# Optimization experiments

Measured on AMD Instinct MI355X. Metric: run time of the kernel, lower is better.

Reference implementation:

```python
import jax, jax.numpy as jnp
import numpy as np

N = 50000
E = 400000
IN_C = 512
HID = 64
OUT_C = 40
H = 4
NEG_SLOPE = 0.2
EPS = 1e-16  # PyG softmax denominator epsilon


def glorot(key, shape, fan_in, fan_out):
    limit = float(np.sqrt(6.0 / (fan_in + fan_out)))
    return jax.random.uniform(key, shape, jnp.float32, -limit, limit)


def setup_inputs() -> dict:
    key = jax.random.key(0)
    ks = jax.random.split(key, 8)
    x = jax.random.normal(ks[0], (N, IN_C), jnp.float32)
    # random edges guaranteed to have src != dst (forward adds exactly one self-loop per node)
    src = jax.random.randint(ks[1], (E,), 0, N)
    off = jax.random.randint(ks[2], (E,), 1, N)
    dst = (src + off) % N
    edge_index = jnp.stack([src, dst], axis=0).astype(jnp.int64)
    W1 = glorot(ks[3], (IN_C, H * HID), IN_C, H * HID)
    b1 = jnp.zeros((H * HID,), jnp.float32)
    W2 = glorot(ks[4], (H * HID, H * OUT_C), H * HID, H * OUT_C)
    b2 = jnp.zeros((OUT_C,), jnp.float32)
    return {"x": x, "edge_index": edge_index, "W1": W1, "b1": b1, "W2": W2, "b2": b2}


def _supergat_layer(x, src, dst, W, b, heads, out_c, concat):
    n = x.shape[0]
    h = (x @ W).reshape(n, heads, out_c)            # [N,H,C]
    x_i = h[dst]                                    # [E',H,C] target
    x_j = h[src]                                    # [E',H,C] source
    # MX attention with return_logits=True inside message(): plain dot-product logits
    alpha = jnp.sum(x_i * x_j, axis=-1)             # [E',H]
    alpha = jax.nn.leaky_relu(alpha, NEG_SLOPE)
    # segment softmax over destination node
    amax = jax.ops.segment_max(alpha, dst, num_segments=n)
    alpha = jnp.exp(alpha - amax[dst])
    denom = jax.ops.segment_sum(alpha, dst, num_segments=n)
    alpha = alpha / (denom[dst] + EPS)
    out = jax.ops.segment_sum(x_j * alpha[:, :, None], dst, num_segments=n)  # [N,H,C]
    if concat:
        out = out.reshape(n, heads * out_c)
    else:
        out = out.mean(axis=1)
    return out + b


def reference(x, edge_index, W1, b1, W2, b2):
    # add_self_loops (input edges contain no self loops by construction)
    loop = jnp.arange(N, dtype=edge_index.dtype)
    src = jnp.concatenate([edge_index[0], loop])
    dst = jnp.concatenate([edge_index[1], loop])
    h = _supergat_layer(x, src, dst, W1, b1, H, HID, concat=True)
    h = jax.nn.elu(h)
    out = _supergat_layer(h, src, dst, W2, b2, H, OUT_C, concat=False)
    logp = jax.nn.log_softmax(out, axis=-1)
    att_loss = jnp.zeros((1,), jnp.float32)  # eval mode: get_attention_loss returns 0
    return logp, att_loss
```

## Files before the change

kernel.cpp:

```cpp
#include <hip/hip_runtime.h>
#include <cstddef>
#include <cstdint>

#define HEADS 4
#define OUTC  40
#define NEG   0.2f
#define EPSV  1e-16f

typedef __bf16 bf16x8 __attribute__((ext_vector_type(8)));
typedef float  floatx4 __attribute__((ext_vector_type(4)));

__device__ __forceinline__ void split_bf16(float a, unsigned& hi, unsigned& lo) {
  unsigned u = __float_as_uint(a);
  hi = u >> 16;
  float hf = __uint_as_float(u & 0xFFFF0000u);
  lo = __float_as_uint(a - hf) >> 16;
}

__device__ __forceinline__ void dma16(const void* g, void* l) {
  __builtin_amdgcn_global_load_lds(
      (const __attribute__((address_space(1))) unsigned int*)g,
      (__attribute__((address_space(3))) unsigned int*)l, 16, 0, 0);
}

__global__ void hist_k(const int* __restrict__ dst, int* __restrict__ cnt, int E) {
  int e = blockIdx.x * blockDim.x + threadIdx.x;
  if (e < E) atomicAdd(&cnt[dst[e]], 1);
}

__global__ __launch_bounds__(1024) void scanA_k(const int* __restrict__ cnt,
                                                int* __restrict__ rp,
                                                int* __restrict__ bsum, int n) {
  __shared__ int sh[1024];
  int i = blockIdx.x * 1024 + threadIdx.x;
  int v = (i < n) ? cnt[i] : 0;
  sh[threadIdx.x] = v;
  __syncthreads();
  for (int d = 1; d < 1024; d <<= 1) {
    int t = (threadIdx.x >= d) ? sh[threadIdx.x - d] : 0;
    __syncthreads();
    sh[threadIdx.x] += t;
    __syncthreads();
  }
  if (i < n) rp[i] = sh[threadIdx.x] - v;
  if (threadIdx.x == 1023) bsum[blockIdx.x] = sh[1023];
}

__global__ void scanC_k(int* __restrict__ rp, const int* __restrict__ bsum,
                        int n, int nb) {
  int i = blockIdx.x * blockDim.x + threadIdx.x;
  if (i < n) {
    int b = i >> 10;
    int off = 0;
    for (int j = 0; j < b; ++j) off += bsum[j];
    rp[i] += off;
  }
  if (i == 0) {
    int tot = 0;
    for (int j = 0; j < nb; ++j) tot += bsum[j];
    rp[n] = tot;
  }
}

__global__ void scatter_k(const int* __restrict__ src, const int* __restrict__ dst,
                          const int* __restrict__ rp, int* __restrict__ cur,
                          int* __restrict__ out, int E) {
  int e = blockIdx.x * blockDim.x + threadIdx.x;
  if (e < E) {
    int d = dst[e];
    int p = rp[d] + atomicAdd(&cur[d], 1);
    out[p] = src[e];
  }
}

__global__ void convW_k(const float* __restrict__ W1, unsigned short* __restrict__ Wh1,
                        unsigned short* __restrict__ Wl1,
                        const float* __restrict__ W2, unsigned short* __restrict__ Wh2,
                        unsigned short* __restrict__ Wl2) {
  int id = blockIdx.x * 256 + threadIdx.x;
  if (id < 256 * 512) {
    int n = id >> 9, k = id & 511;
    unsigned h, l;
    split_bf16(W1[k * 256 + n], h, l);
    Wh1[id] = (unsigned short)h;
    Wl1[id] = (unsigned short)l;
  } else {
    int id2 = id - 256 * 512;
    int n = id2 >> 8, k = id2 & 255;
    int hh = n >> 6, c = n & 63;
    float a = (c < OUTC) ? W2[k * 160 + hh * OUTC + c] : 0.f;
    unsigned h, l;
    split_bf16(a, h, l);
    Wh2[id2] = (unsigned short)h;
    Wl2[id2] = (unsigned short)l;
  }
}

template <bool A_FP32, bool COMPACT>
__global__ __launch_bounds__(256, 3) void gemm_dma(const void* Aptr_h, const void* Aptr_l,
                                                   const unsigned short* __restrict__ Bh,
                                                   const unsigned short* __restrict__ Bl,
                                                   float* __restrict__ C, int M, int K) {
  __shared__ __align__(16) unsigned char lds[49152];
  const int tid = threadIdx.x;
  const int lane = tid & 63;
  const int w = tid >> 6;
  const int wr = w >> 1, wc = w & 1;
  const int row0 = blockIdx.y * 128;
  const int col0 = blockIdx.x * 128;
  const int fr = lane & 15, fq = lane >> 4;
  const int swz8 = fr & 7;
  const int swz4 = (fr & 3) ^ ((fr >> 2) & 1);
  const int srcA8 = (lane & 7) ^ (lane >> 3);
  const int srcB4 = (lane & 3) ^ ((lane >> 2) & 3) ^ ((lane >> 4) & 1);

  floatx4 acc[4][4];
#pragma unroll
  for (int i = 0; i < 4; ++i)
#pragma unroll
    for (int j = 0; j < 4; ++j) acc[i][j] = (floatx4){0.f, 0.f, 0.f, 0.f};

  const float* Af32 = (const float*)Aptr_h;
  const unsigned short* Agh = (const unsigned short*)Aptr_h;
  const unsigned short* Agl = (const unsigned short*)Aptr_l;

#define DMA_A(K0)                                                                   \
  do {                                                                              \
    if (A_FP32) {                                                                   \
      _Pragma("unroll") for (int t = 0; t < 4; ++t) {                               \
        int arow = w * 32 + t * 8 + (lane >> 3);                                    \
        int gr = row0 + arow; gr = gr < M ? gr : M - 1;                             \
        dma16(&Af32[(size_t)gr * K + (K0) + srcA8 * 4],                             \
              lds + (size_t)(w * 32 + t * 8) * 128);                                \
      }                                                                             \
    } else {                                                                        \
      _Pragma("unroll") for (int t = 0; t < 2; ++t) {                               \
        int arow = w * 32 + t * 16 + (lane >> 2);                                   \
        int gr = row0 + arow; gr = gr < M ? gr : M - 1;                             \
        size_t go = (size_t)gr * K + (K0) + srcB4 * 8;                              \
        dma16(&Agh[go], lds + (size_t)(w * 32 + t * 16) * 64);                      \
        dma16(&Agl[go], lds + 8192 + (size_t)(w * 32 + t * 16) * 64);               \
      }                                                                             \
    }                                                                               \
  } while (0)

#define DMA_B(K0, BASE)                                                             \
  do {                                                                              \
    _Pragma("unroll") for (int t = 0; t < 2; ++t) {                                 \
      int nrow = w * 32 + t * 16 + (lane >> 2);                                     \
      size_t go = (size_t)(col0 + nrow) * K + (K0) + srcB4 * 8;                     \
      dma16(&Bh[go], lds + (BASE) + (size_t)(w * 32 + t * 16) * 64);                \
      dma16(&Bl[go], lds + (BASE) + 8192 + (size_t)(w * 32 + t * 16) * 64);         \
    }                                                                               \
  } while (0)

  const int nk = K >> 5;
  DMA_B(0, 16384);
  DMA_A(0);
  asm volatile("" ::: "memory");
  for (int k = 0; k < nk; ++k) {
    const int bbase = 16384 + ((k & 1) << 14);
    if (k + 1 < nk) {
      DMA_B((k + 1) << 5, 16384 + (((k + 1) & 1) << 14));
      asm volatile("s_waitcnt vmcnt(4)" ::: "memory");
    } else {
      asm volatile("s_waitcnt vmcnt(0)" ::: "memory");
    }
    asm volatile("s_barrier" ::: "memory");

    bf16x8 ah[4], al[4], bh[4], bl[4];
#pragma unroll
    for (int i = 0; i < 4; ++i) {
      int arow = wr * 64 + i * 16 + fr;
      if (A_FP32) {
        const unsigned char* pa = lds + (size_t)arow * 128;
        float4 v0 = *(const float4*)(pa + (((fq * 2) ^ swz8) * 16));
        float4 v1 = *(const float4*)(pa + (((fq * 2 + 1) ^ swz8) * 16));
        unsigned u0 = __float_as_uint(v0.x), u1 = __float_as_uint(v0.y);
        unsigned u2 = __float_as_uint(v0.z), u3 = __float_as_uint(v0.w);
        unsigned u4 = __float_as_uint(v1.x), u5 = __float_as_uint(v1.y);
        unsigned u6 = __float_as_uint(v1.z), u7 = __float_as_uint(v1.w);
        uint4 H;
        H.x = (u0 >> 16) | (u1 & 0xFFFF0000u);
        H.y = (u2 >> 16) | (u3 & 0xFFFF0000u);
        H.z = (u4 >> 16) | (u5 & 0xFFFF0000u);
        H.w = (u6 >> 16) | (u7 & 0xFFFF0000u);
        uint4 L;
        L.x = (__float_as_uint(v0.x - __uint_as_float(u0 & 0xFFFF0000u)) >> 16) |
              (__float_as_uint(v0.y - __uint_as_float(u1 & 0xFFFF0000u)) & 0xFFFF0000u);
        L.y = (__float_as_uint(v0.z - __uint_as_float(u2 & 0xFFFF0000u)) >> 16) |
              (__float_as_uint(v0.w - __uint_as_float(u3 & 0xFFFF0000u)) & 0xFFFF0000u);
        L.z = (__float_as_uint(v1.x - __uint_as_float(u4 & 0xFFFF0000u)) >> 16) |
              (__float_as_uint(v1.y - __uint_as_float(u5 & 0xFFFF0000u)) & 0xFFFF0000u);
        L.w = (__float_as_uint(v1.z - __uint_as_float(u6 & 0xFFFF0000u)) >> 16) |
              (__float_as_uint(v1.w - __uint_as_float(u7 & 0xFFFF0000u)) & 0xFFFF0000u);
        ah[i] = *(bf16x8*)&H;
        al[i] = *(bf16x8*)&L;
      } else {
        ah[i] = *(bf16x8*)(lds + (size_t)arow * 64 + ((fq ^ swz4) * 16));
        al[i] = *(bf16x8*)(lds + 8192 + (size_t)arow * 64 + ((fq ^ swz4) * 16));
      }
      int brow = wc * 64 + i * 16 + fr;
      bh[i] = *(bf16x8*)(lds + bbase + (size_t)brow * 64 + ((fq ^ swz4) * 16));
      bl[i] = *(bf16x8*)(lds + bbase + 8192 + (size_t)brow * 64 + ((fq ^ swz4) * 16));
    }
    asm volatile("s_waitcnt lgkmcnt(0)" ::: "memory");
    asm volatile("s_barrier" ::: "memory");
    if (k + 1 < nk) DMA_A((k + 1) << 5);

#pragma unroll
    for (int i = 0; i < 4; ++i)
#pragma unroll
      for (int j = 0; j < 4; ++j) {
        acc[i][j] = __builtin_amdgcn_mfma_f32_16x16x32_bf16(ah[i], bh[j], acc[i][j], 0, 0, 0);
        acc[i][j] = __builtin_amdgcn_mfma_f32_16x16x32_bf16(ah[i], bl[j], acc[i][j], 0, 0, 0);
        acc[i][j] = __builtin_amdgcn_mfma_f32_16x16x32_bf16(al[i], bh[j], acc[i][j], 0, 0, 0);
      }
  }
#undef DMA_A
#undef DMA_B

#pragma unroll
  for (int i = 0; i < 4; ++i) {
    int grow_base = row0 + wr * 64 + i * 16 + fq * 4;
#pragma unroll
    for (int r = 0; r < 4; ++r) {
      int grow = grow_base + r;
      if (grow < M) {
        if (COMPACT) {
          int head = blockIdx.x * 2 + wc;
#pragma unroll
          for (int j = 0; j < 4; ++j) {
            int cc = j * 16 + fr;
            if (cc < OUTC) C[(size_t)grow * 160 + head * OUTC + cc] = acc[i][j][r];
          }
        } else {
#pragma unroll
          for (int j = 0; j < 4; ++j)
            C[(size_t)grow * 256 + col0 + wc * 64 + j * 16 + fr] = acc[i][j][r];
        }
      }
    }
  }
}

__global__ __launch_bounds__(256) void agg1_k(const float* __restrict__ h,
                                              const int* __restrict__ rp,
                                              const int* __restrict__ srt,
                                              const float* __restrict__ b1,
                                              unsigned short* __restrict__ outh,
                                              unsigned short* __restrict__ outl, int Nn) {
  int wv = threadIdx.x >> 6, lane = threadIdx.x & 63;
  int node = blockIdx.x * 4 + wv;
  if (node >= Nn) node = Nn - 1;
  const float4 xi = *(const float4*)&h[(size_t)node * 256 + lane * 4];
  float p = xi.x * xi.x + xi.y * xi.y + xi.z * xi.z + xi.w * xi.w;
  p += __shfl_xor(p, 1); p += __shfl_xor(p, 2); p += __shfl_xor(p, 4); p += __shfl_xor(p, 8);
  float a = p > 0.f ? p : NEG * p;
  float m = a, l = 1.f;
  float4 acc = xi;
  const int e0 = rp[node], e1 = rp[node + 1];
  int e = e0;
  for (; e + 4 <= e1; e += 4) {
    int s0 = srt[e], s1 = srt[e + 1], s2 = srt[e + 2], s3 = srt[e + 3];
    const float4 xj0 = *(const float4*)&h[(size_t)s0 * 256 + lane * 4];
    const float4 xj1 = *(const float4*)&h[(size_t)s1 * 256 + lane * 4];
    const float4 xj2 = *(const float4*)&h[(size_t)s2 * 256 + lane * 4];
    const float4 xj3 = *(const float4*)&h[(size_t)s3 * 256 + lane * 4];
    float q0 = xi.x * xj0.x + xi.y * xj0.y + xi.z * xj0.z + xi.w * xj0.w;
    float q1 = xi.x * xj1.x + xi.y * xj1.y + xi.z * xj1.z + xi.w * xj1.w;
    float q2 = xi.x * xj2.x + xi.y * xj2.y + xi.z * xj2.z + xi.w * xj2.w;
    float q3 = xi.x * xj3.x + xi.y * xj3.y + xi.z * xj3.z + xi.w * xj3.w;
    q0 += __shfl_xor(q0, 1); q1 += __shfl_xor(q1, 1); q2 += __shfl_xor(q2, 1); q3 += __shfl_xor(q3, 1);
    q0 += __shfl_xor(q0, 2); q1 += __shfl_xor(q1, 2); q2 += __shfl_xor(q2, 2); q3 += __shfl_xor(q3, 2);
    q0 += __shfl_xor(q0, 4); q1 += __shfl_xor(q1, 4); q2 += __shfl_xor(q2, 4); q3 += __shfl_xor(q3, 4);
    q0 += __shfl_xor(q0, 8); q1 += __shfl_xor(q1, 8); q2 += __shfl_xor(q2, 8); q3 += __shfl_xor(q3, 8);
    float a0 = q0 > 0.f ? q0 : NEG * q0;
    float a1 = q1 > 0.f ? q1 : NEG * q1;
    float a2 = q2 > 0.f ? q2 : NEG * q2;
    float a3 = q3 > 0.f ? q3 : NEG * q3;
    float nm = fmaxf(fmaxf(m, fmaxf(a0, a1)), fmaxf(a2, a3));
    float sc = __expf(m - nm);
    float w0 = __expf(a0 - nm), w1 = __expf(a1 - nm);
    float w2 = __expf(a2 - nm), w3 = __expf(a3 - nm);
    l = l * sc + w0 + w1 + w2 + w3;
    acc.x = acc.x * sc + w0 * xj0.x + w1 * xj1.x + w2 * xj2.x + w3 * xj3.x;
    acc.y = acc.y * sc + w0 * xj0.y + w1 * xj1.y + w2 * xj2.y + w3 * xj3.y;
    acc.z = acc.z * sc + w0 * xj0.z + w1 * xj1.z + w2 * xj2.z + w3 * xj3.z;
    acc.w = acc.w * sc + w0 * xj0.w + w1 * xj1.w + w2 * xj2.w + w3 * xj3.w;
    m = nm;
  }
  for (; e < e1; ++e) {
    int s = srt[e];
    const float4 xj = *(const float4*)&h[(size_t)s * 256 + lane * 4];
    float q = xi.x * xj.x + xi.y * xj.y + xi.z * xj.z + xi.w * xj.w;
    q += __shfl_xor(q, 1); q += __shfl_xor(q, 2); q += __shfl_xor(q, 4); q += __shfl_xor(q, 8);
    float al = q > 0.f ? q : NEG * q;
    float nm = fmaxf(m, al);
    float sc = __expf(m - nm), wt = __expf(al - nm);
    l = l * sc + wt;
    acc.x = acc.x * sc + wt * xj.x;
    acc.y = acc.y * sc + wt * xj.y;
    acc.z = acc.z * sc + wt * xj.z;
    acc.w = acc.w * sc + wt * xj.w;
    m = nm;
  }
  float inv = 1.f / (l + EPSV);
  const float4 bb = *(const float4*)&b1[lane * 4];
  float4 o;
  o.x = acc.x * inv + bb.x;
  o.y = acc.y * inv + bb.y;
  o.z = acc.z * inv + bb.z;
  o.w = acc.w * inv + bb.w;
  o.x = o.x > 0.f ? o.x : __expf(o.x) - 1.f;
  o.y = o.y > 0.f ? o.y : __expf(o.y) - 1.f;
  o.z = o.z > 0.f ? o.z : __expf(o.z) - 1.f;
  o.w = o.w > 0.f ? o.w : __expf(o.w) - 1.f;
  unsigned h0, l0, h1, l1, h2, l2, h3, l3;
  split_bf16(o.x, h0, l0);
  split_bf16(o.y, h1, l1);
  split_bf16(o.z, h2, l2);
  split_bf16(o.w, h3, l3);
  size_t base = (size_t)node * 256 + lane * 4;
  *(uint2*)&outh[base] = make_uint2(h0 | (h1 << 16), h2 | (h3 << 16));
  *(uint2*)&outl[base] = make_uint2(l0 | (l1 << 16), l2 | (l3 << 16));
}

__global__ __launch_bounds__(256) void agg2_k(const float* __restrict__ h,
                                              const int* __restrict__ rp,
                                              const int* __restrict__ srt,
                                              const float* __restrict__ b2,
                                              float* __restrict__ out, int Nn) {
  __shared__ float buf[4][160];
  int wv = threadIdx.x >> 6, lane = threadIdx.x & 63;
  int node = blockIdx.x * 4 + wv;
  if (node >= Nn) node = Nn - 1;
  const int head = lane >> 4, c4 = lane & 15;
  const bool act = c4 < 10;
  float4 xi = make_float4(0.f, 0.f, 0.f, 0.f);
  if (act) xi = *(const float4*)&h[(size_t)node * 160 + head * OUTC + c4 * 4];
  float p = xi.x * xi.x + xi.y * xi.y + xi.z * xi.z + xi.w * xi.w;
  p += __shfl_xor(p, 1); p += __shfl_xor(p, 2); p += __shfl_xor(p, 4); p += __shfl_xor(p, 8);
  float a = p > 0.f ? p : NEG * p;
  float m = a, l = 1.f;
  float4 acc = xi;
  const int e0 = rp[node], e1 = rp[node + 1];
  int e = e0;
  for (; e + 4 <= e1; e += 4) {
    int s0 = srt[e], s1 = srt[e + 1], s2 = srt[e + 2], s3 = srt[e + 3];
    float4 xj0 = make_float4(0.f, 0.f, 0.f, 0.f);
    float4 xj1 = make_float4(0.f, 0.f, 0.f, 0.f);
    float4 xj2 = make_float4(0.f, 0.f, 0.f, 0.f);
    float4 xj3 = make_float4(0.f, 0.f, 0.f, 0.f);
    if (act) {
      xj0 = *(const float4*)&h[(size_t)s0 * 160 + head * OUTC + c4 * 4];
      xj1 = *(const float4*)&h[(size_t)s1 * 160 + head * OUTC + c4 * 4];
      xj2 = *(const float4*)&h[(size_t)s2 * 160 + head * OUTC + c4 * 4];
      xj3 = *(const float4*)&h[(size_t)s3 * 160 + head * OUTC + c4 * 4];
    }
    float q0 = xi.x * xj0.x + xi.y * xj0.y + xi.z * xj0.z + xi.w * xj0.w;
    float q1 = xi.x * xj1.x + xi.y * xj1.y + xi.z * xj1.z + xi.w * xj1.w;
    float q2 = xi.x * xj2.x + xi.y * xj2.y + xi.z * xj2.z + xi.w * xj2.w;
    float q3 = xi.x * xj3.x + xi.y * xj3.y + xi.z * xj3.z + xi.w * xj3.w;
    q0 += __shfl_xor(q0, 1); q1 += __shfl_xor(q1, 1); q2 += __shfl_xor(q2, 1); q3 += __shfl_xor(q3, 1);
    q0 += __shfl_xor(q0, 2); q1 += __shfl_xor(q1, 2); q2 += __shfl_xor(q2, 2); q3 += __shfl_xor(q3, 2);
    q0 += __shfl_xor(q0, 4); q1 += __shfl_xor(q1, 4); q2 += __shfl_xor(q2, 4); q3 += __shfl_xor(q3, 4);
    q0 += __shfl_xor(q0, 8); q1 += __shfl_xor(q1, 8); q2 += __shfl_xor(q2, 8); q3 += __shfl_xor(q3, 8);
    float a0 = q0 > 0.f ? q0 : NEG * q0;
    float a1 = q1 > 0.f ? q1 : NEG * q1;
    float a2 = q2 > 0.f ? q2 : NEG * q2;
    float a3 = q3 > 0.f ? q3 : NEG * q3;
    float nm = fmaxf(fmaxf(m, fmaxf(a0, a1)), fmaxf(a2, a3));
    float sc = __expf(m - nm);
    float w0 = __expf(a0 - nm), w1 = __expf(a1 - nm);
    float w2 = __expf(a2 - nm), w3 = __expf(a3 - nm);
    l = l * sc + w0 + w1 + w2 + w3;
    acc.x = acc.x * sc + w0 * xj0.x + w1 * xj1.x + w2 * xj2.x + w3 * xj3.x;
    acc.y = acc.y * sc + w0 * xj0.y + w1 * xj1.y + w2 * xj2.y + w3 * xj3.y;
    acc.z = acc.z * sc + w0 * xj0.z + w1 * xj1.z + w2 * xj2.z + w3 * xj3.z;
    acc.w = acc.w * sc + w0 * xj0.w + w1 * xj1.w + w2 * xj2.w + w3 * xj3.w;
    m = nm;
  }
  for (; e < e1; ++e) {
    int s = srt[e];
    float4 xj = make_float4(0.f, 0.f, 0.f, 0.f);
    if (act) xj = *(const float4*)&h[(size_t)s * 160 + head * OUTC + c4 * 4];
    float q = xi.x * xj.x + xi.y * xj.y + xi.z * xj.z + xi.w * xj.w;
    q += __shfl_xor(q, 1); q += __shfl_xor(q, 2); q += __shfl_xor(q, 4); q += __shfl_xor(q, 8);
    float al = q > 0.f ? q : NEG * q;
    float nm = fmaxf(m, al);
    float sc = __expf(m - nm), wt = __expf(al - nm);
    l = l * sc + wt;
    acc.x = acc.x * sc + wt * xj.x;
    acc.y = acc.y * sc + wt * xj.y;
    acc.z = acc.z * sc + wt * xj.z;
    acc.w = acc.w * sc + wt * xj.w;
    m = nm;
  }
  float inv = 1.f / (l + EPSV);
  if (act) {
    float4 res;
    res.x = acc.x * inv; res.y = acc.y * inv; res.z = acc.z * inv; res.w = acc.w * inv;
    *(float4*)&buf[wv][head * OUTC + c4 * 4] = res;
  }
  __syncthreads();
  const bool valid = lane < OUTC;
  float v = 0.f;
  if (valid)
    v = 0.25f * (buf[wv][lane] + buf[wv][OUTC + lane] + buf[wv][2 * OUTC + lane] +
                 buf[wv][3 * OUTC + lane]) + b2[lane];
  float t = valid ? v : -1e30f;
#pragma unroll
  for (int off = 32; off; off >>= 1) t = fmaxf(t, __shfl_xor(t, off));
  float ex = valid ? __expf(v - t) : 0.f;
  float s = ex;
#pragma unroll
  for (int off = 32; off; off >>= 1) s += __shfl_xor(s, off);
  float lse = t + __logf(s);
  if (valid) out[(size_t)node * OUTC + lane] = v - lse;
  if (blockIdx.x == 0 && threadIdx.x == 0) out[(size_t)Nn * OUTC] = 0.f;
}

extern "C" void kernel_launch(void* const* d_in, const int* in_sizes, int n_in,
                              void* d_out, int out_size, void* d_ws, size_t ws_size,
                              hipStream_t stream) {
  const float* x  = (const float*)d_in[0];
  const int*   ei = (const int*)d_in[1];
  const float* W1 = (const float*)d_in[2];
  const float* b1 = (const float*)d_in[3];
  const float* W2 = (const float*)d_in[4];
  const float* b2 = (const float*)d_in[5];
  float* out = (float*)d_out;

  const int Nn = in_sizes[0] / 512;
  const int E  = in_sizes[1] / 2;
  const int* esrc = ei;
  const int* edst = ei + E;
  const int NB = (Nn + 1023) / 1024;

  char* ws = (char*)d_ws;
  const size_t szH = (size_t)Nn * 256 * sizeof(float);
  float* h1 = (float*)(ws);
  size_t off = szH;
  unsigned short* g1h = (unsigned short*)(ws + off); off += (size_t)Nn * 256 * 2;
  unsigned short* g1l = (unsigned short*)(ws + off); off += (size_t)Nn * 256 * 2;
  int* rp = (int*)(ws + off);   off += ((size_t)(Nn + 1) * 4 + 15) & ~(size_t)15;
  int* cnt = (int*)(ws + off);  off += ((size_t)Nn * 4 + 15) & ~(size_t)15;
  int* srt = (int*)(ws + off);  off += ((size_t)E * 4 + 15) & ~(size_t)15;
  int* bsum = (int*)(ws + off); off += 1024;
  unsigned short* Wh1 = (unsigned short*)(ws + off); off += (size_t)256 * 512 * 2;
  unsigned short* Wl1 = (unsigned short*)(ws + off); off += (size_t)256 * 512 * 2;
  unsigned short* Wh2 = (unsigned short*)(ws + off); off += (size_t)256 * 256 * 2;
  unsigned short* Wl2 = (unsigned short*)(ws + off); off += (size_t)256 * 256 * 2;
  float* h2 = h1;

  hipMemsetAsync(cnt, 0, (size_t)Nn * sizeof(int), stream);
  hist_k<<<(E + 255) / 256, 256, 0, stream>>>(edst, cnt, E);
  scanA_k<<<NB, 1024, 0, stream>>>(cnt, rp, bsum, Nn);
  scanC_k<<<(Nn + 255) / 256, 256, 0, stream>>>(rp, bsum, Nn, NB);
  hipMemsetAsync(cnt, 0, (size_t)Nn * sizeof(int), stream);
  scatter_k<<<(E + 255) / 256, 256, 0, stream>>>(esrc, edst, rp, cnt, srt, E);

  convW_k<<<768, 256, 0, stream>>>(W1, Wh1, Wl1, W2, Wh2, Wl2);

  gemm_dma<true, false>
      <<<dim3(2, (Nn + 127) / 128), 256, 0, stream>>>(x, nullptr, Wh1, Wl1, h1, Nn, 512);
  agg1_k<<<(Nn + 3) / 4, 256, 0, stream>>>(h1, rp, srt, b1, g1h, g1l, Nn);

  gemm_dma<false, true>
      <<<dim3(2, (Nn + 127) / 128), 256, 0, stream>>>(g1h, g1l, Wh2, Wl2, h2, Nn, 256);
  agg2_k<<<(Nn + 3) / 4, 256, 0, stream>>>(h2, rp, srt, b2, out, Nn);
}
```

Baseline: 394.0 us.

## Single-buffer B low half in GEMM to fit four blocks per CU; fuse cnt reset

The GEMM's shared-memory footprint drops from 48KB to 40KB. Only the high bf16 half of the B tile stays double-buffered; the low half gets one buffer that is refilled alongside A after the fragment-read barrier. This allows launch bounds of 4 blocks per CU instead of 3, trading some load/compute overlap for more occupancy. Separately, the second memset of the count array is folded into the scan-offset kernel, removing one launch.

```diff
diff --git a/kernel.cpp b/kernel.cpp
--- a/kernel.cpp
+++ b/kernel.cpp
@@ -47,13 +47,14 @@
 }
 
 __global__ void scanC_k(int* __restrict__ rp, const int* __restrict__ bsum,
-                        int n, int nb) {
+                        int* __restrict__ cnt, int n, int nb) {
   int i = blockIdx.x * blockDim.x + threadIdx.x;
   if (i < n) {
     int b = i >> 10;
     int off = 0;
     for (int j = 0; j < b; ++j) off += bsum[j];
     rp[i] += off;
+    cnt[i] = 0;
   }
   if (i == 0) {
     int tot = 0;
@@ -97,11 +98,11 @@
 }
 
 template <bool A_FP32, bool COMPACT>
-__global__ __launch_bounds__(256, 3) void gemm_dma(const void* Aptr_h, const void* Aptr_l,
+__global__ __launch_bounds__(256, 4) void gemm_dma(const void* Aptr_h, const void* Aptr_l,
                                                    const unsigned short* __restrict__ Bh,
                                                    const unsigned short* __restrict__ Bl,
                                                    float* __restrict__ C, int M, int K) {
-  __shared__ __align__(16) unsigned char lds[49152];
+  __shared__ __align__(16) unsigned char lds[40960];
   const int tid = threadIdx.x;
   const int lane = tid & 63;
   const int w = tid >> 6;
@@ -144,25 +145,34 @@
     }                                                                               \
   } while (0)
 
-#define DMA_B(K0, BASE)                                                             \
+#define DMA_BHI(K0, BASE)                                                           \
   do {                                                                              \
     _Pragma("unroll") for (int t = 0; t < 2; ++t) {                                 \
       int nrow = w * 32 + t * 16 + (lane >> 2);                                     \
       size_t go = (size_t)(col0 + nrow) * K + (K0) + srcB4 * 8;                     \
       dma16(&Bh[go], lds + (BASE) + (size_t)(w * 32 + t * 16) * 64);                \
-      dma16(&Bl[go], lds + (BASE) + 8192 + (size_t)(w * 32 + t * 16) * 64);         \
     }                                                                               \
   } while (0)
 
+#define DMA_BLO(K0)                                                                 \
+  do {                                                                              \
+    _Pragma("unroll") for (int t = 0; t < 2; ++t) {                                 \
+      int nrow = w * 32 + t * 16 + (lane >> 2);                                     \
+      size_t go = (size_t)(col0 + nrow) * K + (K0) + srcB4 * 8;                     \
+      dma16(&Bl[go], lds + 32768 + (size_t)(w * 32 + t * 16) * 64);                 \
+    }                                                                               \
+  } while (0)
+
   const int nk = K >> 5;
-  DMA_B(0, 16384);
+  DMA_BHI(0, 16384);
   DMA_A(0);
+  DMA_BLO(0);
   asm volatile("" ::: "memory");
   for (int k = 0; k < nk; ++k) {
-    const int bbase = 16384 + ((k & 1) << 14);
+    const int bbase = 16384 + ((k & 1) << 13);
     if (k + 1 < nk) {
-      DMA_B((k + 1) << 5, 16384 + (((k + 1) & 1) << 14));
-      asm volatile("s_waitcnt vmcnt(4)" ::: "memory");
+      DMA_BHI((k + 1) << 5, 16384 + (((k + 1) & 1) << 13));
+      asm volatile("s_waitcnt vmcnt(2)" ::: "memory");
     } else {
       asm volatile("s_waitcnt vmcnt(0)" ::: "memory");
     }
@@ -202,11 +212,14 @@
       }
       int brow = wc * 64 + i * 16 + fr;
       bh[i] = *(bf16x8*)(lds + bbase + (size_t)brow * 64 + ((fq ^ swz4) * 16));
-      bl[i] = *(bf16x8*)(lds + bbase + 8192 + (size_t)brow * 64 + ((fq ^ swz4) * 16));
+      bl[i] = *(bf16x8*)(lds + 32768 + (size_t)brow * 64 + ((fq ^ swz4) * 16));
     }
     asm volatile("s_waitcnt lgkmcnt(0)" ::: "memory");
     asm volatile("s_barrier" ::: "memory");
-    if (k + 1 < nk) DMA_A((k + 1) << 5);
+    if (k + 1 < nk) {
+      DMA_A((k + 1) << 5);
+      DMA_BLO((k + 1) << 5);
+    }
 
 #pragma unroll
     for (int i = 0; i < 4; ++i)
@@ -218,7 +231,8 @@
       }
   }
 #undef DMA_A
-#undef DMA_B
+#undef DMA_BHI
+#undef DMA_BLO
 
 #pragma unroll
   for (int i = 0; i < 4; ++i) {
@@ -457,8 +471,7 @@
   hipMemsetAsync(cnt, 0, (size_t)Nn * sizeof(int), stream);
   hist_k<<<(E + 255) / 256, 256, 0, stream>>>(edst, cnt, E);
   scanA_k<<<NB, 1024, 0, stream>>>(cnt, rp, bsum, Nn);
-  scanC_k<<<(Nn + 255) / 256, 256, 0, stream>>>(rp, bsum, Nn, NB);
-  hipMemsetAsync(cnt, 0, (size_t)Nn * sizeof(int), stream);
+  scanC_k<<<(Nn + 255) / 256, 256, 0, stream>>>(rp, bsum, cnt, Nn, NB);
   scatter_k<<<(E + 255) / 256, 256, 0, stream>>>(esrc, edst, rp, cnt, srt, E);
 
   convW_k<<<768, 256, 0, stream>>>(W1, Wh1, Wl1, W2, Wh2, Wl2);
```

Result: slower. 582.3 us (+47.8%).
